# Optimization experiments

Hardware: AMD Instinct MI355X
Metric: run time of the kernel (lower is better)

Reference implementation:

```python
import jax, jax.numpy as jnp
import numpy as np

B, T, D_IN = 8, 1024, 320
L, H, DK, DV, DM, DI = 6, 8, 64, 64, 512, 2048


def _pe_table():
    pos = np.arange(T, dtype=np.float32)[:, None]
    div = np.exp(np.arange(0, DM, 2, dtype=np.float32) * (-np.log(10000.0) / DM))
    pe = np.zeros((T, DM), np.float32)
    pe[:, 0::2] = np.sin(pos * div)
    pe[:, 1::2] = np.cos(pos * div)
    return jnp.asarray(pe)


def setup_inputs() -> dict:
    key = jax.random.key(0)
    ks = jax.random.split(key, 16)
    rn = lambda k, shape, std: (jax.random.normal(k, shape, jnp.float32) * std)
    inp = {}
    inp["padded_input"] = jax.random.normal(ks[0], (B, T, D_IN), jnp.float32)
    inp["input_lengths"] = jax.random.randint(ks[1], (B,), T // 2, T + 1)
    # input projection + input layernorm (weights stored as [in, out])
    inp["w_in"] = rn(ks[2], (D_IN, DM), 0.02)
    inp["b_in"] = jnp.zeros((DM,), jnp.float32)
    inp["ln_in_g"] = jnp.ones((DM,), jnp.float32)
    inp["ln_in_b"] = jnp.zeros((DM,), jnp.float32)
    inp["pe"] = _pe_table()
    # stacked per-layer params, leading dim L
    inp["wq"] = rn(ks[3], (L, DM, H * DK), np.sqrt(2.0 / (DM + DK)))
    inp["bq"] = jnp.zeros((L, H * DK), jnp.float32)
    inp["wk"] = rn(ks[4], (L, DM, H * DK), np.sqrt(2.0 / (DM + DK)))
    inp["bk"] = jnp.zeros((L, H * DK), jnp.float32)
    inp["wv"] = rn(ks[5], (L, DM, H * DV), np.sqrt(2.0 / (DM + DV)))
    inp["bv"] = jnp.zeros((L, H * DV), jnp.float32)
    inp["wfc"] = rn(ks[6], (L, H * DV, DM), np.sqrt(2.0 / (H * DV + DM)))
    inp["bfc"] = jnp.zeros((L, DM), jnp.float32)
    inp["ln1_g"] = jnp.ones((L, DM), jnp.float32)
    inp["ln1_b"] = jnp.zeros((L, DM), jnp.float32)
    inp["w1"] = rn(ks[7], (L, DM, DI), np.sqrt(2.0 / (DM + DI)))
    inp["b1"] = jnp.zeros((L, DI), jnp.float32)
    inp["w2"] = rn(ks[8], (L, DI, DM), np.sqrt(2.0 / (DM + DI)))
    inp["b2"] = jnp.zeros((L, DM), jnp.float32)
    inp["ln2_g"] = jnp.ones((L, DM), jnp.float32)
    inp["ln2_b"] = jnp.zeros((L, DM), jnp.float32)
    return inp


def _layer_norm(x, g, b):
    mu = jnp.mean(x, axis=-1, keepdims=True)
    var = jnp.var(x, axis=-1, keepdims=True)
    return (x - mu) * jax.lax.rsqrt(var + 1e-5) * g + b


def _encoder(padded_input, input_lengths, w_in, b_in, ln_in_g, ln_in_b, pe,
             wq, bq, wk, bk, wv, bv, wfc, bfc, ln1_g, ln1_b,
             w1, b1, w2, b2, ln2_g, ln2_b):
    pos = jnp.arange(T)
    key_pad = pos[None, :] >= input_lengths[:, None]          # [B,T] True at pad
    non_pad = (~key_pad).astype(padded_input.dtype)[:, :, None]  # [B,T,1]
    scale = 1.0 / jnp.sqrt(jnp.float32(DK))

    x = _layer_norm(padded_input @ w_in + b_in, ln_in_g, ln_in_b) + pe[None]

    def body(x, p):
        Wq, Bq, Wk, Bk, Wv, Bv, Wfc, Bfc, G1, Bn1, W1, Bf1, W2, Bf2, G2, Bn2 = p
        res = x
        q = (x @ Wq + Bq).reshape(B, T, H, DK)
        k = (x @ Wk + Bk).reshape(B, T, H, DK)
        v = (x @ Wv + Bv).reshape(B, T, H, DV)
        attn = jnp.einsum('bqhd,bkhd->bhqk', q, k) * scale
        attn = jnp.where(key_pad[:, None, None, :], -jnp.inf, attn)
        attn = jax.nn.softmax(attn, axis=-1)
        o = jnp.einsum('bhqk,bkhd->bqhd', attn, v).reshape(B, T, H * DV)
        x = _layer_norm(o @ Wfc + Bfc + res, G1, Bn1) * non_pad
        res = x
        h = jax.nn.relu(x @ W1 + Bf1)
        x = _layer_norm(h @ W2 + Bf2 + res, G2, Bn2) * non_pad
        return x, None

    x, _ = jax.lax.scan(body, x, (wq, bq, wk, bk, wv, bv, wfc, bfc,
                                  ln1_g, ln1_b, w1, b1, w2, b2, ln2_g, ln2_b))
    return x


def reference(padded_input, input_lengths, w_in, b_in, ln_in_g, ln_in_b, pe,
              wq, bq, wk, bk, wv, bv, wfc, bfc, ln1_g, ln1_b,
              w1, b1, w2, b2, ln2_g, ln2_b):
    # dropout is identity in eval mode
    return _encoder(padded_input, input_lengths, w_in, b_in, ln_in_g, ln_in_b, pe,
                    wq, bq, wk, bk, wv, bv, wfc, bfc, ln1_g, ln1_b,
                    w1, b1, w2, b2, ln2_g, ln2_b)
```

## Files before the change

kernel.cpp:

```cpp
#include <hip/hip_runtime.h>
#include <hip/hip_bf16.h>


typedef unsigned short bh16;
typedef __bf16 bf16x8 __attribute__((ext_vector_type(8)));
typedef float f32x4 __attribute__((ext_vector_type(4)));
typedef unsigned int u32x4 __attribute__((ext_vector_type(4)));
typedef unsigned int u32x2 __attribute__((ext_vector_type(2)));

#define DEVI static __device__ __forceinline__

DEVI bh16 f2bf(float f) {
  union { float f; unsigned u; } x; x.f = f;
  unsigned r = x.u + 0x7fffu + ((x.u >> 16) & 1u);
  return (bh16)(r >> 16);
}
DEVI float bf2f(bh16 u) {
  union { unsigned u; float f; } x; x.u = ((unsigned)u) << 16; return x.f;
}
DEVI bf16x8 ld16(const bh16* p) {
  return __builtin_bit_cast(bf16x8, *(const u32x4*)p);
}
DEVI bf16x8 ld16b(const char* p) {
  return __builtin_bit_cast(bf16x8, *(const u32x4*)p);
}
DEVI f32x4 mfma16(bf16x8 a, bf16x8 b, f32x4 c) {
  return __builtin_amdgcn_mfma_f32_16x16x32_bf16(a, b, c, 0, 0, 0);
}
DEVI void async16(const void* g, void* l) {
  __builtin_amdgcn_global_load_lds(
      (const __attribute__((address_space(1))) void*)g,
      (__attribute__((address_space(3))) void*)l, 16, 0, 0);
}

__global__ __launch_bounds__(256) void tcvt(
    const float* __restrict__ in, bh16* __restrict__ out,
    int K, int N, long long inLS, long long outLS, int rowOff) {
  int l = blockIdx.z;
  in += (size_t)l * inLS;
  out += (size_t)l * outLS + (size_t)rowOff * K;
  __shared__ float t[32][33];
  int n0 = blockIdx.x * 32, k0 = blockIdx.y * 32;
  int tx = threadIdx.x & 31, ty = threadIdx.x >> 5;
#pragma unroll
  for (int i = 0; i < 4; i++)
    t[ty + 8 * i][tx] = in[(size_t)(k0 + ty + 8 * i) * N + n0 + tx];
  __syncthreads();
#pragma unroll
  for (int i = 0; i < 4; i++)
    out[(size_t)(n0 + ty + 8 * i) * K + k0 + tx] = f2bf(t[tx][ty + 8 * i]);
}

__global__ __launch_bounds__(256) void bcat(
    const float* __restrict__ bq, const float* __restrict__ bk,
    const float* __restrict__ bv, float* __restrict__ out) {
  int l = blockIdx.x;
  for (int j = threadIdx.x; j < 1536; j += 256) {
    float v = (j < 512) ? bq[l * 512 + j]
            : (j < 1024) ? bk[l * 512 + j - 512] : bv[l * 512 + j - 1024];
    out[l * 1536 + j] = v;
  }
}

__global__ __launch_bounds__(256) void cvt_in(
    const float* __restrict__ in, bh16* __restrict__ out, int n4) {
  int i = blockIdx.x * 256 + threadIdx.x;
  if (i < n4) {
    float4 v = ((const float4*)in)[i];
    u32x2 pk;
    pk[0] = (unsigned)f2bf(v.x) | ((unsigned)f2bf(v.y) << 16);
    pk[1] = (unsigned)f2bf(v.z) | ((unsigned)f2bf(v.w) << 16);
    *(u32x2*)(out + (size_t)i * 4) = pk;
  }
}

template <int BM, int BN, int RELU, int OUTF32, int QKV>
__global__ __launch_bounds__(256, 2) void gemm_bt(
    const bh16* __restrict__ A, const bh16* __restrict__ Bt,
    const float* __restrict__ bias, void* __restrict__ Cout,
    bh16* __restrict__ vtOut, int M, int N, int K) {
  constexpr int BK = 64;
  __shared__ __align__(16) bh16 As[BM * BK];
  __shared__ __align__(16) bh16 Bs[BN * BK];
  const int tid = threadIdx.x;
  const int wave = tid >> 6, lane = tid & 63;
  const int lq = lane & 15, grp = lane >> 4;
  const int p = blockIdx.x;
  const int xcd = p & 7, idx = p >> 3;
  const int m0 = (((xcd << 3) | (idx & 7))) * BM;
  const int n0 = (idx >> 3) * BN;
  constexpr int FM = BM / 32, FN = BN / 32;
  const int wr = wave >> 1, wc = wave & 1;
  f32x4 acc[FM][FN] = {};

  const int nk = K / BK;
  for (int kt = 0; kt < nk; ++kt) {
#pragma unroll
    for (int i = 0; i < BM / 32; ++i) {
      int off = i * 4096 + wave * 1024 + lane * 16;
      int row = off >> 7, col = off & 127;
      const char* g = (const char*)A + ((size_t)(m0 + row) * K + kt * BK) * 2 + col;
      async16(g, (char*)As + off);
    }
#pragma unroll
    for (int i = 0; i < BN / 32; ++i) {
      int off = i * 4096 + wave * 1024 + lane * 16;
      int row = off >> 7, col = off & 127;
      const char* g = (const char*)Bt + ((size_t)(n0 + row) * K + kt * BK) * 2 + col;
      async16(g, (char*)Bs + off);
    }
    __syncthreads();
#pragma unroll
    for (int kk = 0; kk < 2; ++kk) {
      bf16x8 af[FM], bfr[FN];
#pragma unroll
      for (int i = 0; i < FM; ++i) {
        int row = wr * (BM / 2) + i * 16 + lq;
        af[i] = ld16(As + row * BK + kk * 32 + grp * 8);
      }
#pragma unroll
      for (int j = 0; j < FN; ++j) {
        int row = wc * (BN / 2) + j * 16 + lq;
        bfr[j] = ld16(Bs + row * BK + kk * 32 + grp * 8);
      }
#pragma unroll
      for (int i = 0; i < FM; ++i)
#pragma unroll
        for (int j = 0; j < FN; ++j)
          acc[i][j] = mfma16(af[i], bfr[j], acc[i][j]);
    }
    __syncthreads();
  }
  if (QKV && n0 >= 1024) {
#pragma unroll
    for (int i = 0; i < FM; ++i) {
#pragma unroll
      for (int j = 0; j < FN; ++j) {
        int col = n0 + wc * (BN / 2) + j * 16 + lq;
        float bv = bias[col];
        int vc = col - 1024;
        int t0 = m0 + wr * (BM / 2) + i * 16 + grp * 4;
        int bb = t0 >> 10, tl = t0 & 1023;
        u32x2 pk;
        pk[0] = (unsigned)f2bf(acc[i][j][0] + bv) |
                ((unsigned)f2bf(acc[i][j][1] + bv) << 16);
        pk[1] = (unsigned)f2bf(acc[i][j][2] + bv) |
                ((unsigned)f2bf(acc[i][j][3] + bv) << 16);
        *(u32x2*)&vtOut[((size_t)(bb * 512 + vc)) * 1024 + tl] = pk;
      }
    }
    return;
  }
#pragma unroll
  for (int i = 0; i < FM; ++i) {
#pragma unroll
    for (int j = 0; j < FN; ++j) {
      int col = n0 + wc * (BN / 2) + j * 16 + lq;
      float bv = bias[col];
#pragma unroll
      for (int r = 0; r < 4; ++r) {
        int row = m0 + wr * (BM / 2) + i * 16 + grp * 4 + r;
        float v = acc[i][j][r] + bv;
        if (RELU) v = fmaxf(v, 0.f);
        if (OUTF32) ((float*)Cout)[(size_t)row * N + col] = v;
        else ((bh16*)Cout)[(size_t)row * N + col] = f2bf(v);
      }
    }
  }
}

__global__ __launch_bounds__(256) void ln_pe_k(
    const float* __restrict__ in, const float* __restrict__ g,
    const float* __restrict__ bta, const float* __restrict__ pe,
    float* __restrict__ xf, bh16* __restrict__ xb) {
  int wave = threadIdx.x >> 6, lane = threadIdx.x & 63;
  int row = blockIdx.x * 4 + wave;
  int t = row & 1023;
  const float* xr = in + (size_t)row * 512 + lane * 8;
  float4 a0 = ((const float4*)xr)[0], a1 = ((const float4*)xr)[1];
  float v[8] = {a0.x, a0.y, a0.z, a0.w, a1.x, a1.y, a1.z, a1.w};
  float s = 0.f, ss = 0.f;
#pragma unroll
  for (int j = 0; j < 8; j++) { s += v[j]; ss += v[j] * v[j]; }
#pragma unroll
  for (int m = 1; m < 64; m <<= 1) { s += __shfl_xor(s, m); ss += __shfl_xor(ss, m); }
  float mu = s * (1.f / 512.f);
  float rstd = rsqrtf(ss * (1.f / 512.f) - mu * mu + 1e-5f);
  int c0 = lane * 8;
  float o[8];
  u32x4 pk;
#pragma unroll
  for (int j = 0; j < 8; j++) {
    int c = c0 + j;
    o[j] = (v[j] - mu) * rstd * g[c] + bta[c] + pe[(size_t)t * 512 + c];
  }
  float4* xo = (float4*)(xf + (size_t)row * 512 + c0);
  xo[0] = make_float4(o[0], o[1], o[2], o[3]);
  xo[1] = make_float4(o[4], o[5], o[6], o[7]);
#pragma unroll
  for (int j = 0; j < 4; j++)
    pk[j] = (unsigned)f2bf(o[2 * j]) | ((unsigned)f2bf(o[2 * j + 1]) << 16);
  *(u32x4*)(xb + (size_t)row * 512 + c0) = pk;
}

__global__ __launch_bounds__(256) void ln_res_k(
    const bh16* __restrict__ gout, const float* __restrict__ res,
    const float* __restrict__ g, const float* __restrict__ bta,
    const int* __restrict__ lens,
    float* __restrict__ xf, bh16* __restrict__ xb) {
  int wave = threadIdx.x >> 6, lane = threadIdx.x & 63;
  int row = blockIdx.x * 4 + wave;
  int b = row >> 10, t = row & 1023;
  float nonpad = (t < lens[b]) ? 1.f : 0.f;
  int c0 = lane * 8;
  u32x4 graw = *(const u32x4*)(gout + (size_t)row * 512 + c0);
  const float* rr = res + (size_t)row * 512 + c0;
  float4 r0 = ((const float4*)rr)[0], r1 = ((const float4*)rr)[1];
  float v[8];
#pragma unroll
  for (int j = 0; j < 4; j++) {
    v[2 * j] = bf2f((bh16)(graw[j] & 0xffffu));
    v[2 * j + 1] = bf2f((bh16)(graw[j] >> 16));
  }
  v[0] += r0.x; v[1] += r0.y; v[2] += r0.z; v[3] += r0.w;
  v[4] += r1.x; v[5] += r1.y; v[6] += r1.z; v[7] += r1.w;
  float s = 0.f, ss = 0.f;
#pragma unroll
  for (int j = 0; j < 8; j++) { s += v[j]; ss += v[j] * v[j]; }
#pragma unroll
  for (int m = 1; m < 64; m <<= 1) { s += __shfl_xor(s, m); ss += __shfl_xor(ss, m); }
  float mu = s * (1.f / 512.f);
  float rstd = rsqrtf(ss * (1.f / 512.f) - mu * mu + 1e-5f);
  float o[8];
  u32x4 pk;
#pragma unroll
  for (int j = 0; j < 8; j++) {
    int c = c0 + j;
    o[j] = ((v[j] - mu) * rstd * g[c] + bta[c]) * nonpad;
  }
  float4* xo = (float4*)(xf + (size_t)row * 512 + c0);
  xo[0] = make_float4(o[0], o[1], o[2], o[3]);
  xo[1] = make_float4(o[4], o[5], o[6], o[7]);
#pragma unroll
  for (int j = 0; j < 4; j++)
    pk[j] = (unsigned)f2bf(o[2 * j]) | ((unsigned)f2bf(o[2 * j + 1]) << 16);
  *(u32x4*)(xb + (size_t)row * 512 + c0) = pk;
}

__global__ __launch_bounds__(512) void attn_k(
    const bh16* __restrict__ qkv, const bh16* __restrict__ vt,
    const int* __restrict__ lens, bh16* __restrict__ o) {
  constexpr int LDP = 72;
  __shared__ __align__(16) char Ks[2][8192];
  __shared__ __align__(16) char Vs[2][8192];
  __shared__ __align__(16) bh16 P[8][16 * LDP];
  int p = blockIdx.x;
  int xcd = p & 7, s = p >> 3;
  int bh = ((s & 7) << 3) | xcd;
  int qt = s >> 3;
  int b = bh >> 3, h = bh & 7;
  int len = lens[b];
  if (qt * 128 >= len) return;
  int tid = threadIdx.x;
  int wave = tid >> 6, lane = tid & 63;
  int lq = lane & 15, grp = lane >> 4;

  size_t qrow = (size_t)(b * 1024 + qt * 128 + wave * 16 + lq);
  const bh16* Qp = qkv + qrow * 1536 + h * 64;
  bf16x8 qf0 = ld16(Qp + grp * 8);
  bf16x8 qf1 = ld16(Qp + 32 + grp * 8);
  const char* Kbase = (const char*)(qkv + (size_t)(b * 1024) * 1536 + 512 + h * 64);
  const char* Vbase = (const char*)(vt + (size_t)(bh * 64) * 1024);
  bh16* Pw = P[wave];

  f32x4 oacc[4] = {};
  float m = -1e30f, lsum = 0.f;
  int nkb = (len + 63) >> 6;

  auto stage = [&](int buf, int kb) {
    int off = tid * 16;
    int row = off >> 7, cb = off & 127;
    int sw = (row & 7) << 4;
    async16(Kbase + (size_t)(kb * 64 + row) * 3072 + (cb ^ sw), Ks[buf] + off);
    async16(Vbase + (size_t)row * 2048 + kb * 128 + (cb ^ sw), Vs[buf] + off);
  };

  stage(0, 0);
  for (int kb = 0; kb < nkb; ++kb) {
    int cur = kb & 1;
    __syncthreads();
    if (kb + 1 < nkb) stage(cur ^ 1, kb + 1);
    int k64 = kb * 64;
    f32x4 st[4];
    __builtin_amdgcn_s_setprio(1);
#pragma unroll
    for (int sv = 0; sv < 4; ++sv) {
      int row = sv * 16 + lq, sw = (row & 7) << 4;
      const char* kp = Ks[cur] + row * 128;
      f32x4 z = {};
      z = mfma16(ld16b(kp + ((grp * 16) ^ sw)), qf0, z);
      z = mfma16(ld16b(kp + ((64 + grp * 16) ^ sw)), qf1, z);
      st[sv] = z;
    }
    __builtin_amdgcn_s_setprio(0);
    float tmax = -1e30f;
    if (k64 + 64 > len) {
#pragma unroll
      for (int sv = 0; sv < 4; ++sv)
#pragma unroll
        for (int r = 0; r < 4; ++r) {
          int key = k64 + sv * 16 + grp * 4 + r;
          float v = st[sv][r] * 0.125f;
          v = (key < len) ? v : -1e30f;
          st[sv][r] = v;
          tmax = fmaxf(tmax, v);
        }
    } else {
#pragma unroll
      for (int sv = 0; sv < 4; ++sv)
#pragma unroll
        for (int r = 0; r < 4; ++r) {
          float v = st[sv][r] * 0.125f;
          st[sv][r] = v;
          tmax = fmaxf(tmax, v);
        }
    }
    tmax = fmaxf(tmax, __shfl_xor(tmax, 16));
    tmax = fmaxf(tmax, __shfl_xor(tmax, 32));
    float newm = fmaxf(m, tmax);
    if (!__all(newm - m <= 8.f)) {
      float sc = __expf(m - newm);
      m = newm;
      lsum *= sc;
#pragma unroll
      for (int r = 0; r < 4; ++r) {
        float scr = __shfl(sc, grp * 4 + r);
#pragma unroll
        for (int dt = 0; dt < 4; ++dt) oacc[dt][r] *= scr;
      }
    }
    float rs = 0.f;
#pragma unroll
    for (int sv = 0; sv < 4; ++sv) {
      float p0 = __expf(st[sv][0] - m), p1 = __expf(st[sv][1] - m);
      float p2 = __expf(st[sv][2] - m), p3 = __expf(st[sv][3] - m);
      rs += (p0 + p1) + (p2 + p3);
      u32x2 pk;
      pk[0] = (unsigned)f2bf(p0) | ((unsigned)f2bf(p1) << 16);
      pk[1] = (unsigned)f2bf(p2) | ((unsigned)f2bf(p3) << 16);
      *(u32x2*)&Pw[lq * LDP + sv * 16 + grp * 4] = pk;
    }
    rs += __shfl_xor(rs, 16);
    rs += __shfl_xor(rs, 32);
    lsum += rs;
#pragma unroll
    for (int kk = 0; kk < 2; ++kk) {
      bf16x8 pa = ld16(Pw + lq * LDP + kk * 32 + grp * 8);
      __builtin_amdgcn_s_setprio(1);
#pragma unroll
      for (int dt = 0; dt < 4; ++dt) {
        int row = dt * 16 + lq, sw = (row & 7) << 4;
        bf16x8 vfr = ld16b(Vs[cur] + row * 128 + ((kk * 64 + grp * 16) ^ sw));
        oacc[dt] = mfma16(pa, vfr, oacc[dt]);
      }
      __builtin_amdgcn_s_setprio(0);
    }
  }
#pragma unroll
  for (int r = 0; r < 4; ++r) {
    float li = __shfl(lsum, grp * 4 + r);
    float inv = 1.f / li;
    int row = qt * 128 + wave * 16 + grp * 4 + r;
    bh16* orow = o + (size_t)(b * 1024 + row) * 512 + h * 64;
#pragma unroll
    for (int dt = 0; dt < 4; ++dt) orow[dt * 16 + lq] = f2bf(oacc[dt][r] * inv);
  }
}

extern "C" void kernel_launch(void* const* d_in, const int* in_sizes, int n_in,
                              void* d_out, int out_size, void* d_ws, size_t ws_size,
                              hipStream_t stream) {
  const float* padded = (const float*)d_in[0];
  const int* lens = (const int*)d_in[1];
  const float* w_in = (const float*)d_in[2];
  const float* b_in = (const float*)d_in[3];
  const float* ln_in_g = (const float*)d_in[4];
  const float* ln_in_b = (const float*)d_in[5];
  const float* pe = (const float*)d_in[6];
  const float* wq = (const float*)d_in[7];
  const float* bq = (const float*)d_in[8];
  const float* wk = (const float*)d_in[9];
  const float* bk = (const float*)d_in[10];
  const float* wv = (const float*)d_in[11];
  const float* bv = (const float*)d_in[12];
  const float* wfc = (const float*)d_in[13];
  const float* bfc = (const float*)d_in[14];
  const float* ln1_g = (const float*)d_in[15];
  const float* ln1_b = (const float*)d_in[16];
  const float* w1 = (const float*)d_in[17];
  const float* b1 = (const float*)d_in[18];
  const float* w2 = (const float*)d_in[19];
  const float* b2 = (const float*)d_in[20];
  const float* ln2_g = (const float*)d_in[21];
  const float* ln2_b = (const float*)d_in[22];

  char* ws = (char*)d_ws;
  size_t off = 0;
  auto alloc = [&](size_t bytes) -> char* {
    char* p = ws + off;
    off += (bytes + 255) & ~(size_t)255;
    return p;
  };
  bh16* WinT  = (bh16*)alloc((size_t)512 * 320 * 2);
  bh16* WqkvT = (bh16*)alloc((size_t)6 * 1536 * 512 * 2);
  bh16* WfcT  = (bh16*)alloc((size_t)6 * 512 * 512 * 2);
  bh16* W1T   = (bh16*)alloc((size_t)6 * 2048 * 512 * 2);
  bh16* W2T   = (bh16*)alloc((size_t)6 * 512 * 2048 * 2);
  float* bqkv = (float*)alloc((size_t)6 * 1536 * 4);
  bh16* xb    = (bh16*)alloc((size_t)8192 * 512 * 2);
  float* xf   = (float*)alloc((size_t)8192 * 512 * 4);
  bh16* qkvb  = (bh16*)alloc((size_t)8192 * 1536 * 2);
  bh16* vt    = (bh16*)alloc((size_t)64 * 64 * 1024 * 2);
  bh16* ob    = (bh16*)alloc((size_t)8192 * 512 * 2);
  float* tmp32 = (float*)alloc((size_t)8192 * 512 * 4);
  bh16* tmp16 = (bh16*)alloc((size_t)8192 * 512 * 2);
  bh16* hbuf  = (bh16*)alloc((size_t)8192 * 2048 * 2);
  bh16* padb  = hbuf;
  if (off > ws_size) return;

  tcvt<<<dim3(16, 10, 1), 256, 0, stream>>>(w_in, WinT, 320, 512, 0, 0, 0);
  tcvt<<<dim3(16, 16, 6), 256, 0, stream>>>(wq, WqkvT, 512, 512, 512 * 512, 1536 * 512, 0);
  tcvt<<<dim3(16, 16, 6), 256, 0, stream>>>(wk, WqkvT, 512, 512, 512 * 512, 1536 * 512, 512);
  tcvt<<<dim3(16, 16, 6), 256, 0, stream>>>(wv, WqkvT, 512, 512, 512 * 512, 1536 * 512, 1024);
  tcvt<<<dim3(16, 16, 6), 256, 0, stream>>>(wfc, WfcT, 512, 512, 512 * 512, 512 * 512, 0);
  tcvt<<<dim3(64, 16, 6), 256, 0, stream>>>(w1, W1T, 512, 2048, (long long)512 * 2048, (long long)2048 * 512, 0);
  tcvt<<<dim3(16, 64, 6), 256, 0, stream>>>(w2, W2T, 2048, 512, (long long)2048 * 512, (long long)512 * 2048, 0);
  bcat<<<6, 256, 0, stream>>>(bq, bk, bv, bqkv);
  cvt_in<<<2560, 256, 0, stream>>>(padded, padb, 655360);

  gemm_bt<128, 64, 0, 1, 0><<<512, 256, 0, stream>>>(
      padb, WinT, b_in, tmp32, nullptr, 8192, 512, 320);
  ln_pe_k<<<2048, 256, 0, stream>>>(tmp32, ln_in_g, ln_in_b, pe, xf, xb);

  for (int l = 0; l < 6; ++l) {
    gemm_bt<128, 128, 0, 0, 1><<<768, 256, 0, stream>>>(
        xb, WqkvT + (size_t)l * 1536 * 512, bqkv + l * 1536, qkvb, vt,
        8192, 1536, 512);
    attn_k<<<512, 512, 0, stream>>>(qkvb, vt, lens, ob);
    gemm_bt<128, 64, 0, 0, 0><<<512, 256, 0, stream>>>(
        ob, WfcT + (size_t)l * 512 * 512, bfc + l * 512, tmp16, nullptr,
        8192, 512, 512);
    ln_res_k<<<2048, 256, 0, stream>>>(tmp16, xf, ln1_g + l * 512, ln1_b + l * 512,
                                       lens, xf, xb);
    gemm_bt<128, 128, 1, 0, 0><<<1024, 256, 0, stream>>>(
        xb, W1T + (size_t)l * 2048 * 512, b1 + l * 2048, hbuf, nullptr,
        8192, 2048, 512);
    gemm_bt<128, 64, 0, 0, 0><<<512, 256, 0, stream>>>(
        hbuf, W2T + (size_t)l * 512 * 2048, b2 + l * 512, tmp16, nullptr,
        8192, 512, 2048);
    float* xfo = (l == 5) ? (float*)d_out : xf;
    ln_res_k<<<2048, 256, 0, stream>>>(tmp16, xf, ln2_g + l * 512, ln2_b + l * 512,
                                       lens, xfo, xb);
  }
}
```

Before: 941.6 us.

## Double-buffer GEMM LDS tiles and XOR-swizzle them to avoid bank conflicts

```diff
diff --git a/kernel.cpp b/kernel.cpp
--- a/kernel.cpp
+++ b/kernel.cpp
@@ -75,13 +75,13 @@
 }
 
 template <int BM, int BN, int RELU, int OUTF32, int QKV>
-__global__ __launch_bounds__(256, 2) void gemm_bt(
+__global__ __launch_bounds__(256) void gemm_bt(
     const bh16* __restrict__ A, const bh16* __restrict__ Bt,
     const float* __restrict__ bias, void* __restrict__ Cout,
     bh16* __restrict__ vtOut, int M, int N, int K) {
   constexpr int BK = 64;
-  __shared__ __align__(16) bh16 As[BM * BK];
-  __shared__ __align__(16) bh16 Bs[BN * BK];
+  __shared__ __align__(16) bh16 As[2][BM * BK];
+  __shared__ __align__(16) bh16 Bs[2][BN * BK];
   const int tid = threadIdx.x;
   const int wave = tid >> 6, lane = tid & 63;
   const int lq = lane & 15, grp = lane >> 4;
@@ -94,34 +94,46 @@
   f32x4 acc[FM][FN] = {};
 
   const int nk = K / BK;
-  for (int kt = 0; kt < nk; ++kt) {
+  auto stage = [&](int buf, int kt) {
 #pragma unroll
     for (int i = 0; i < BM / 32; ++i) {
       int off = i * 4096 + wave * 1024 + lane * 16;
       int row = off >> 7, col = off & 127;
-      const char* g = (const char*)A + ((size_t)(m0 + row) * K + kt * BK) * 2 + col;
-      async16(g, (char*)As + off);
+      int sw = (row & 7) << 4;
+      const char* g =
+          (const char*)A + ((size_t)(m0 + row) * K + kt * BK) * 2 + (col ^ sw);
+      async16(g, (char*)As[buf] + off);
     }
 #pragma unroll
     for (int i = 0; i < BN / 32; ++i) {
       int off = i * 4096 + wave * 1024 + lane * 16;
       int row = off >> 7, col = off & 127;
-      const char* g = (const char*)Bt + ((size_t)(n0 + row) * K + kt * BK) * 2 + col;
-      async16(g, (char*)Bs + off);
-    }
+      int sw = (row & 7) << 4;
+      const char* g =
+          (const char*)Bt + ((size_t)(n0 + row) * K + kt * BK) * 2 + (col ^ sw);
+      async16(g, (char*)Bs[buf] + off);
+    }
+  };
+
+  stage(0, 0);
+  for (int kt = 0; kt < nk; ++kt) {
+    int cur = kt & 1;
     __syncthreads();
+    if (kt + 1 < nk) stage(cur ^ 1, kt + 1);
 #pragma unroll
     for (int kk = 0; kk < 2; ++kk) {
       bf16x8 af[FM], bfr[FN];
 #pragma unroll
       for (int i = 0; i < FM; ++i) {
         int row = wr * (BM / 2) + i * 16 + lq;
-        af[i] = ld16(As + row * BK + kk * 32 + grp * 8);
+        int sw = (row & 7) << 4;
+        af[i] = ld16b((char*)As[cur] + row * 128 + ((kk * 64 + grp * 16) ^ sw));
       }
 #pragma unroll
       for (int j = 0; j < FN; ++j) {
         int row = wc * (BN / 2) + j * 16 + lq;
-        bfr[j] = ld16(Bs + row * BK + kk * 32 + grp * 8);
+        int sw = (row & 7) << 4;
+        bfr[j] = ld16b((char*)Bs[cur] + row * 128 + ((kk * 64 + grp * 16) ^ sw));
       }
 #pragma unroll
       for (int i = 0; i < FM; ++i)
@@ -129,7 +141,6 @@
         for (int j = 0; j < FN; ++j)
           acc[i][j] = mfma16(af[i], bfr[j], acc[i][j]);
     }
-    __syncthreads();
   }
   if (QKV && n0 >= 1024) {
 #pragma unroll
```

After: 859.1 us. 8.8% less time.
